# Optimization experiments

Hardware: AMD Instinct MI355X
Metric: run time of the kernel (lower is better)

## Reference

```python
import jax, jax.numpy as jnp
import numpy as np

H = 1024
E = 8
TOP_K = 2


def setup_inputs() -> dict:
    key = jax.random.key(0)
    ks = jax.random.split(key, 6)
    B, S = 4, 2048
    hidden_states = jax.random.normal(ks[0], (B, S, H), dtype=jnp.float32)
    # router weight, init N(0, 0.02)
    router_w = jax.random.normal(ks[1], (E, H), dtype=jnp.float32) * 0.02
    # stacked expert FFN params (nn.Linear: y = x @ W.T + b)
    lim = 1.0 / np.sqrt(H)
    W1 = jax.random.uniform(ks[2], (E, H, H), minval=-lim, maxval=lim, dtype=jnp.float32)
    b1 = jax.random.uniform(ks[3], (E, H), minval=-lim, maxval=lim, dtype=jnp.float32)
    W2 = jax.random.uniform(ks[4], (E, H, H), minval=-lim, maxval=lim, dtype=jnp.float32)
    b2 = jax.random.uniform(ks[5], (E, H), minval=-lim, maxval=lim, dtype=jnp.float32)
    return {"hidden_states": hidden_states, "router_w": router_w,
            "W1": W1, "b1": b1, "W2": W2, "b2": b2}


def reference(hidden_states, router_w, W1, b1, W2, b2):
    B, S, _ = hidden_states.shape
    # ---- router ----
    logits = jnp.einsum('bsh,eh->bse', hidden_states, router_w)  # [B,S,E]
    router_probs = jax.nn.softmax(logits.astype(jnp.float32), axis=-1)
    top_vals, top_idx = jax.lax.top_k(router_probs, TOP_K)        # [B,S,K]
    top_vals = top_vals / jnp.sum(top_vals, axis=-1, keepdims=True)  # norm_topk_prob
    # per-token per-expert combine weight (sum of top-k weights matching expert)
    w = jnp.sum(jax.nn.one_hot(top_idx, E, dtype=top_vals.dtype) * top_vals[..., None], axis=-2)  # [B,S,E]
    # ---- dense all-expert FFN (faithful to reference: every expert on every token) ----
    h1 = jax.nn.relu(jnp.einsum('bsh,efh->bsef', hidden_states, W1) + b1)   # [B,S,E,F]
    expert_out = jnp.einsum('bsef,egf->bseg', h1, W2) + b2                  # [B,S,E,H]
    moe_out = jnp.einsum('bseh,bse->bsh', expert_out, w)
    return hidden_states + moe_out, router_probs
```

## Files before the change

### kernel.cpp

```cpp
#include <hip/hip_runtime.h>
#include <hip/hip_bf16.h>


#define HD   1024
#define NTOK 8192
#define NEXP 8
#define BM   128
#define BN   256
#define BK   32
#define ZROW 8192
#define MAXP 17408
#define EP_LDSW 136

typedef __attribute__((ext_vector_type(8))) short  vshort8;
typedef __attribute__((ext_vector_type(4))) short  vshort4;
typedef __attribute__((ext_vector_type(4))) float  vfloat4;

typedef __attribute__((address_space(1))) const unsigned gas_uint;
typedef __attribute__((address_space(3))) unsigned       las_uint;

__device__ __forceinline__ void gld16(const void* g, void* l) {
    __builtin_amdgcn_global_load_lds((gas_uint*)g, (las_uint*)l, 16, 0, 0);
}

__device__ __forceinline__ short bf16r(float f) {
    union { float f; unsigned u; } a; a.f = f;
    unsigned r = a.u + 0x7FFFu + ((a.u >> 16) & 1u);
    return (short)(r >> 16);
}

__global__ void init_kernel(int* counts, int* fill, int* pair_token, short* xb) {
    int i = blockIdx.x * 256 + threadIdx.x;
    if (i < NEXP) { counts[i] = 0; fill[i] = 0; }
    if (i < MAXP) pair_token[i] = ZROW;
    if (i < HD / 8) {
        vshort8 z = {0, 0, 0, 0, 0, 0, 0, 0};
        *(vshort8*)(xb + (size_t)ZROW * HD + i * 8) = z;
    }
}

__global__ __launch_bounds__(256) void router_kernel(
    const float* __restrict__ x, const float* __restrict__ rw,
    float* __restrict__ out, short* __restrict__ xb,
    float* __restrict__ probs_out, int2* __restrict__ tok_top,
    float2* __restrict__ tok_w, int* __restrict__ counts) {
    __shared__ float rws[NEXP * HD];
    __shared__ int hist[NEXP];
    int t = threadIdx.x;
    if (t < NEXP) hist[t] = 0;
    for (int j = 0; j < 8; ++j) {
        int idx = j * 1024 + t * 4;
        *(vfloat4*)(rws + idx) = *(const vfloat4*)(rw + idx);
    }
    __syncthreads();
    int wave = t >> 6, lane = t & 63;
    for (int it = 0; it < 8; ++it) {
        int token = blockIdx.x * 32 + it * 4 + wave;
        const float* xr = x + (size_t)token * HD;
        float part[NEXP];
#pragma unroll
        for (int e = 0; e < NEXP; ++e) part[e] = 0.f;
        for (int j = 0; j < 4; ++j) {
            int off = j * 256 + lane * 4;
            vfloat4 xv = *(const vfloat4*)(xr + off);
            *(vfloat4*)(out + (size_t)token * HD + off) = xv;
            vshort4 bq;
            bq.x = bf16r(xv.x); bq.y = bf16r(xv.y); bq.z = bf16r(xv.z); bq.w = bf16r(xv.w);
            *(vshort4*)(xb + (size_t)token * HD + off) = bq;
#pragma unroll
            for (int e = 0; e < NEXP; ++e) {
                vfloat4 wv = *(const vfloat4*)(rws + e * HD + off);
                part[e] += xv.x * wv.x + xv.y * wv.y + xv.z * wv.z + xv.w * wv.w;
            }
        }
#pragma unroll
        for (int e = 0; e < NEXP; ++e)
            for (int off = 32; off; off >>= 1)
                part[e] += __shfl_xor(part[e], off, 64);
        if (lane == 0) {
            float m = part[0];
#pragma unroll
            for (int e = 1; e < NEXP; ++e) m = fmaxf(m, part[e]);
            float p[NEXP], s = 0.f;
#pragma unroll
            for (int e = 0; e < NEXP; ++e) { p[e] = expf(part[e] - m); s += p[e]; }
            float inv = 1.f / s;
#pragma unroll
            for (int e = 0; e < NEXP; ++e) {
                p[e] *= inv;
                probs_out[(size_t)token * NEXP + e] = p[e];
            }
            int i0 = 0;
#pragma unroll
            for (int e = 1; e < NEXP; ++e) if (p[e] > p[i0]) i0 = e;
            int i1 = (i0 == 0) ? 1 : 0;
#pragma unroll
            for (int e = 0; e < NEXP; ++e) if (e != i0 && p[e] > p[i1]) i1 = e;
            float s2 = 1.f / (p[i0] + p[i1]);
            tok_top[token] = make_int2(i0, i1);
            tok_w[token]   = make_float2(p[i0] * s2, p[i1] * s2);
            atomicAdd(&hist[i0], 1);
            atomicAdd(&hist[i1], 1);
        }
    }
    __syncthreads();
    if (t < NEXP) atomicAdd(&counts[t], hist[t]);
}

__global__ __launch_bounds__(256) void scatter_kernel(
    const int2* __restrict__ tok_top, const float2* __restrict__ tok_w,
    const int* __restrict__ counts, int* fill,
    int* __restrict__ pair_token, float* __restrict__ pair_w) {
    __shared__ int lhist[NEXP];
    __shared__ int lbase[NEXP];
    int t = threadIdx.x;
    if (t < NEXP) lhist[t] = 0;
    __syncthreads();
    int offs[NEXP];
    {
        int acc = 0;
#pragma unroll
        for (int f = 0; f < NEXP; ++f) {
            offs[f] = acc;
            acc += (counts[f] + 127) & ~127;
        }
    }
    int token = blockIdx.x * 256 + t;
    int2 ti = tok_top[token];
    float2 tw = tok_w[token];
    int r0 = atomicAdd(&lhist[ti.x], 1);
    int r1 = atomicAdd(&lhist[ti.y], 1);
    __syncthreads();
    if (t < NEXP) lbase[t] = atomicAdd(&fill[t], lhist[t]);
    __syncthreads();
    int s0 = offs[ti.x] + lbase[ti.x] + r0;
    pair_token[s0] = token; pair_w[s0] = tw.x;
    int s1 = offs[ti.y] + lbase[ti.y] + r1;
    pair_token[s1] = token; pair_w[s1] = tw.y;
}

__global__ void convw_kernel(const float* __restrict__ W1, const float* __restrict__ W2,
                             short* __restrict__ D1, short* __restrict__ D2) {
    size_t t = (size_t)blockIdx.x * 256 + threadIdx.x;
    const size_t PER = (size_t)NEXP * HD * HD / 8;
    const float* src = W1; short* dst = D1;
    if (t >= PER) { t -= PER; src = W2; dst = D2; }
    size_t C = t >> 6;
    int l  = (int)(t & 63);
    int kc = (int)(C & 31);
    int ng = (int)((C >> 5) & 63);
    int ei = (int)(C >> 11);
    int n = ng * 16 + (l & 15);
    int k = kc * 32 + (l >> 4) * 8;
    const float* s = src + ((size_t)ei * HD + n) * HD + k;
    vfloat4 a = *(const vfloat4*)s;
    vfloat4 b = *(const vfloat4*)(s + 4);
    vshort8 o;
    o[0] = bf16r(a.x); o[1] = bf16r(a.y); o[2] = bf16r(a.z); o[3] = bf16r(a.w);
    o[4] = bf16r(b.x); o[5] = bf16r(b.y); o[6] = bf16r(b.z); o[7] = bf16r(b.w);
    *(vshort8*)(dst + t * 8) = o;
}

template <int MODE>
__global__ __launch_bounds__(512, 4) void moe_gemm(
    const short* __restrict__ A, const short* __restrict__ Bw,
    const float* __restrict__ bias, const int* __restrict__ pair_token,
    const float* __restrict__ pair_w, const int* __restrict__ counts,
    short* __restrict__ h1sw_out, float* __restrict__ out) {
    __shared__ short smem[24576];

    const int row0 = blockIdx.x * BM;
    int e = 0;
    {
        int csum = 0;
#pragma unroll
        for (int f = 0; f < NEXP; ++f) {
            int p = (counts[f] + 127) & ~127;
            if (csum + p <= row0) e = f + 1;
            csum += p;
        }
        if (row0 >= csum) return;
    }

    const int t = threadIdx.x;
    const int wave = t >> 6, lane = t & 63;
    const int wm = wave >> 2, wn = wave & 3;
    const int quad = lane >> 4, l16 = lane & 15;
    const int colb = blockIdx.y * BN;

    const char* agp;
    if (MODE == 0) {
        int tok = pair_token[row0 + wave * 16 + l16];
        agp = (const char*)A + (size_t)tok * (HD * 2) + quad * 16;
    } else {
        agp = (const char*)A + ((size_t)(row0 >> 4) + wave) * 32768 + lane * 16;
    }
    const char* bgp = (const char*)Bw +
        ((size_t)e * 64 + (colb >> 4) + 2 * wave) * 32768 + lane * 16;

    vfloat4 acc[4][4];
#pragma unroll
    for (int i = 0; i < 4; ++i)
#pragma unroll
        for (int j = 0; j < 4; ++j)
            acc[i][j] = (vfloat4){0.f, 0.f, 0.f, 0.f};

#define STAGE(bsel, kt_)                                                      \
    {                                                                         \
        short* sa_ = smem + (bsel) * 4096;                                    \
        short* sb_ = smem + 8192 + (bsel) * 8192;                             \
        const char* ga_ = (MODE == 0)                                         \
            ? (agp + (size_t)(kt_) * 64)                                      \
            : (agp + (size_t)(kt_) * 1024);                                   \
        gld16(ga_, sa_ + wave * 512);                                         \
        gld16(bgp + (size_t)(kt_) * 1024,         sb_ + (2 * wave) * 512);    \
        gld16(bgp + 32768 + (size_t)(kt_) * 1024, sb_ + (2 * wave + 1) * 512);\
    }

    STAGE(0, 0)
    int cur = 0;
    for (int kt = 0; kt < HD / BK; ++kt) {
        if (kt < HD / BK - 1) {
            STAGE(cur ^ 1, kt + 1)
            asm volatile("s_waitcnt vmcnt(3)" ::: "memory");
        } else {
            asm volatile("s_waitcnt vmcnt(0)" ::: "memory");
        }
        __builtin_amdgcn_s_barrier();
        asm volatile("" ::: "memory");
        const short* sa = smem + cur * 4096;
        const short* sb = smem + 8192 + cur * 8192;
        vshort8 af[4], bfr[4];
#pragma unroll
        for (int i = 0; i < 4; ++i)
            af[i] = *(const vshort8*)(sa + (wm * 4 + i) * 512 + lane * 8);
#pragma unroll
        for (int j = 0; j < 4; ++j)
            bfr[j] = *(const vshort8*)(sb + (wn * 4 + j) * 512 + lane * 8);
#pragma unroll
        for (int i = 0; i < 4; ++i)
#pragma unroll
            for (int j = 0; j < 4; ++j)
                acc[i][j] = __builtin_amdgcn_mfma_f32_16x16x32_bf16(af[i], bfr[j], acc[i][j], 0, 0, 0);
        asm volatile("" ::: "memory");
        __builtin_amdgcn_s_barrier();
        cur ^= 1;
    }
#undef STAGE

    if (MODE == 0) {
        __syncthreads();
#pragma unroll
        for (int h = 0; h < 2; ++h) {
            if ((wn >> 1) == h) {
#pragma unroll
                for (int j = 0; j < 4; ++j) {
                    int col = (wn & 1) * 64 + j * 16 + l16;
                    float bv = bias[e * HD + colb + h * 128 + col];
#pragma unroll
                    for (int i = 0; i < 4; ++i) {
                        int rl = wm * 64 + i * 16 + quad * 4;
#pragma unroll
                        for (int reg = 0; reg < 4; ++reg) {
                            float v = acc[i][j][reg] + bv;
                            v = v > 0.f ? v : 0.f;
                            smem[(rl + reg) * EP_LDSW + col] = bf16r(v);
                        }
                    }
                }
            }
            __syncthreads();
            int lrow = wave * 16 + l16;
#pragma unroll
            for (int kk = 0; kk < 4; ++kk) {
                vshort8 v = *(const vshort8*)(smem + lrow * EP_LDSW + kk * 32 + quad * 8);
                size_t chunk = ((size_t)((row0 >> 4) + wave) * 32) + (colb >> 5) + h * 4 + kk;
                *(vshort8*)(h1sw_out + chunk * 512 + lane * 8) = v;
            }
            if (h == 0) __syncthreads();
        }
    } else {
        int tok[4][4]; float wv[4][4];
#pragma unroll
        for (int i = 0; i < 4; ++i)
#pragma unroll
            for (int reg = 0; reg < 4; ++reg) {
                int r = row0 + wm * 64 + i * 16 + quad * 4 + reg;
                tok[i][reg] = pair_token[r];
                wv[i][reg] = pair_w[r];
            }
#pragma unroll
        for (int j = 0; j < 4; ++j) {
            int col = colb + wn * 64 + j * 16 + l16;
            float bv = bias[e * HD + col];
#pragma unroll
            for (int i = 0; i < 4; ++i)
#pragma unroll
                for (int reg = 0; reg < 4; ++reg)
                    if (tok[i][reg] < ZROW)
                        atomicAdd(out + (size_t)tok[i][reg] * HD + col,
                                  wv[i][reg] * (acc[i][j][reg] + bv));
        }
    }
}

extern "C" void kernel_launch(void* const* d_in, const int* in_sizes, int n_in,
                              void* d_out, int out_size, void* d_ws, size_t ws_size,
                              hipStream_t stream) {
    const float* x  = (const float*)d_in[0];
    const float* rw = (const float*)d_in[1];
    const float* W1 = (const float*)d_in[2];
    const float* b1 = (const float*)d_in[3];
    const float* W2 = (const float*)d_in[4];
    const float* b2 = (const float*)d_in[5];
    float* out   = (float*)d_out;
    float* probs = out + (size_t)NTOK * HD;

    char* ws = (char*)d_ws;
    short* xb = (short*)ws;            ws += (size_t)(NTOK + 1) * HD * 2;
    short* h1 = (short*)ws;            ws += (size_t)MAXP * HD * 2;
    int*   pair_token = (int*)ws;      ws += MAXP * 4;
    float* pair_w     = (float*)ws;    ws += MAXP * 4;
    int*   counts = (int*)ws;          ws += 256;
    int*   fill   = (int*)ws;          ws += 256;
    int2*   tok_top = (int2*)ws;       ws += NTOK * 8;
    float2* tok_w   = (float2*)ws;     ws += NTOK * 8;
    short* w1sw = (short*)ws;          ws += (size_t)NEXP * HD * HD * 2;
    short* w2sw = (short*)ws;          ws += (size_t)NEXP * HD * HD * 2;
    (void)ws_size;

    init_kernel<<<MAXP / 256, 256, 0, stream>>>(counts, fill, pair_token, xb);
    router_kernel<<<NTOK / 32, 256, 0, stream>>>(x, rw, out, xb, probs,
                                                 tok_top, tok_w, counts);
    scatter_kernel<<<NTOK / 256, 256, 0, stream>>>(tok_top, tok_w, counts, fill,
                                                   pair_token, pair_w);
    int cg = (int)(2 * ((size_t)NEXP * HD * HD / 8) / 256);
    convw_kernel<<<cg, 256, 0, stream>>>(W1, W2, w1sw, w2sw);
    dim3 gg(MAXP / BM, HD / BN);
    moe_gemm<0><<<gg, 512, 0, stream>>>(xb, w1sw, b1, pair_token, pair_w, counts, h1, nullptr);
    moe_gemm<1><<<gg, 512, 0, stream>>>(h1, w2sw, b2, pair_token, pair_w, counts, nullptr, out);
}
```

Baseline: 313.0 us.

## Shrink GEMM tile to 128x128 with 4 waves and triple-buffered LDS register prefetch

Changes the MoE GEMM tile from 128x256 with 8 waves to 128x128 with 4 waves, so each wave now stages two A and two B chunks per k-step. The main loop becomes a three-buffer LDS pipeline unrolled by six, with register double-buffered fragments: fragments for the next k-step are read from LDS while the MFMAs for the current step run, and there is one barrier per step instead of two. The aim is to hide LDS and global latency and to double the number of column blocks for better occupancy. The trade-off is lower B reuse per block, more A traffic, and manual pipeline bookkeeping that depends on the fixed 32 k-steps.

```diff
diff --git a/kernel.cpp b/kernel.cpp
--- a/kernel.cpp
+++ b/kernel.cpp
@@ -6,7 +6,7 @@
 #define NTOK 8192
 #define NEXP 8
 #define BM   128
-#define BN   256
+#define BN   128
 #define BK   32
 #define ZROW 8192
 #define MAXP 17408
@@ -162,7 +162,7 @@
 }
 
 template <int MODE>
-__global__ __launch_bounds__(512, 4) void moe_gemm(
+__global__ __launch_bounds__(256, 3) void moe_gemm(
     const short* __restrict__ A, const short* __restrict__ Bw,
     const float* __restrict__ bias, const int* __restrict__ pair_token,
     const float* __restrict__ pair_w, const int* __restrict__ counts,
@@ -184,19 +184,23 @@
 
     const int t = threadIdx.x;
     const int wave = t >> 6, lane = t & 63;
-    const int wm = wave >> 2, wn = wave & 3;
+    const int wm = wave >> 1, wn = wave & 1;
     const int quad = lane >> 4, l16 = lane & 15;
     const int colb = blockIdx.y * BN;
 
-    const char* agp;
+    const char *agp0, *agp1;
     if (MODE == 0) {
-        int tok = pair_token[row0 + wave * 16 + l16];
-        agp = (const char*)A + (size_t)tok * (HD * 2) + quad * 16;
+        int tok0 = pair_token[row0 + (2 * wave) * 16 + l16];
+        int tok1 = pair_token[row0 + (2 * wave + 1) * 16 + l16];
+        agp0 = (const char*)A + (size_t)tok0 * (HD * 2) + quad * 16;
+        agp1 = (const char*)A + (size_t)tok1 * (HD * 2) + quad * 16;
     } else {
-        agp = (const char*)A + ((size_t)(row0 >> 4) + wave) * 32768 + lane * 16;
-    }
-    const char* bgp = (const char*)Bw +
+        agp0 = (const char*)A + ((size_t)(row0 >> 4) + 2 * wave) * 32768 + lane * 16;
+        agp1 = (const char*)A + ((size_t)(row0 >> 4) + 2 * wave + 1) * 32768 + lane * 16;
+    }
+    const char* bgp0 = (const char*)Bw +
         ((size_t)e * 64 + (colb >> 4) + 2 * wave) * 32768 + lane * 16;
+    const char* bgp1 = bgp0 + 32768;
 
     vfloat4 acc[4][4];
 #pragma unroll
@@ -205,79 +209,103 @@
         for (int j = 0; j < 4; ++j)
             acc[i][j] = (vfloat4){0.f, 0.f, 0.f, 0.f};
 
+    vshort8 afA[4], bfA[4], afB[4], bfB[4];
+
 #define STAGE(bsel, kt_)                                                      \
     {                                                                         \
-        short* sa_ = smem + (bsel) * 4096;                                    \
-        short* sb_ = smem + 8192 + (bsel) * 8192;                             \
-        const char* ga_ = (MODE == 0)                                         \
-            ? (agp + (size_t)(kt_) * 64)                                      \
-            : (agp + (size_t)(kt_) * 1024);                                   \
-        gld16(ga_, sa_ + wave * 512);                                         \
-        gld16(bgp + (size_t)(kt_) * 1024,         sb_ + (2 * wave) * 512);    \
-        gld16(bgp + 32768 + (size_t)(kt_) * 1024, sb_ + (2 * wave + 1) * 512);\
+        short* s_ = smem + (bsel) * 8192;                                     \
+        const char* a0_ = (MODE == 0) ? (agp0 + (size_t)(kt_) * 64)           \
+                                      : (agp0 + (size_t)(kt_) * 1024);        \
+        const char* a1_ = (MODE == 0) ? (agp1 + (size_t)(kt_) * 64)           \
+                                      : (agp1 + (size_t)(kt_) * 1024);        \
+        gld16(a0_, s_ + (2 * wave) * 512);                                    \
+        gld16(a1_, s_ + (2 * wave + 1) * 512);                                \
+        gld16(bgp0 + (size_t)(kt_) * 1024, s_ + 4096 + (2 * wave) * 512);     \
+        gld16(bgp1 + (size_t)(kt_) * 1024, s_ + 4096 + (2 * wave + 1) * 512); \
+    }
+
+#define LOADFRAGS(af_, bf_, bsel)                                             \
+    {                                                                         \
+        const short* sa_ = smem + (bsel) * 8192;                              \
+        _Pragma("unroll")                                                     \
+        for (int i = 0; i < 4; ++i)                                           \
+            af_[i] = *(const vshort8*)(sa_ + (wm * 4 + i) * 512 + lane * 8);  \
+        _Pragma("unroll")                                                     \
+        for (int j = 0; j < 4; ++j)                                           \
+            bf_[j] = *(const vshort8*)(sa_ + 4096 + (wn * 4 + j) * 512 + lane * 8); \
+    }
+
+#define DOMFMA(af_, bf_)                                                      \
+    {                                                                         \
+        _Pragma("unroll")                                                     \
+        for (int i = 0; i < 4; ++i)                                           \
+            _Pragma("unroll")                                                 \
+            for (int j = 0; j < 4; ++j)                                       \
+                acc[i][j] = __builtin_amdgcn_mfma_f32_16x16x32_bf16(          \
+                    af_[i], bf_[j], acc[i][j], 0, 0, 0);                      \
+    }
+
+#define BODY(sbuf, rbuf, ktp2, AFc, BFc, AFr, BFr)                            \
+    {                                                                         \
+        STAGE(sbuf, ktp2)                                                     \
+        asm volatile("s_waitcnt vmcnt(4) lgkmcnt(0)" ::: "memory");           \
+        __builtin_amdgcn_s_barrier();                                         \
+        LOADFRAGS(AFr, BFr, rbuf)                                             \
+        DOMFMA(AFc, BFc)                                                      \
     }
 
     STAGE(0, 0)
-    int cur = 0;
-    for (int kt = 0; kt < HD / BK; ++kt) {
-        if (kt < HD / BK - 1) {
-            STAGE(cur ^ 1, kt + 1)
-            asm volatile("s_waitcnt vmcnt(3)" ::: "memory");
-        } else {
-            asm volatile("s_waitcnt vmcnt(0)" ::: "memory");
-        }
-        __builtin_amdgcn_s_barrier();
-        asm volatile("" ::: "memory");
-        const short* sa = smem + cur * 4096;
-        const short* sb = smem + 8192 + cur * 8192;
-        vshort8 af[4], bfr[4];
-#pragma unroll
-        for (int i = 0; i < 4; ++i)
-            af[i] = *(const vshort8*)(sa + (wm * 4 + i) * 512 + lane * 8);
-#pragma unroll
-        for (int j = 0; j < 4; ++j)
-            bfr[j] = *(const vshort8*)(sb + (wn * 4 + j) * 512 + lane * 8);
-#pragma unroll
-        for (int i = 0; i < 4; ++i)
-#pragma unroll
-            for (int j = 0; j < 4; ++j)
-                acc[i][j] = __builtin_amdgcn_mfma_f32_16x16x32_bf16(af[i], bfr[j], acc[i][j], 0, 0, 0);
-        asm volatile("" ::: "memory");
-        __builtin_amdgcn_s_barrier();
-        cur ^= 1;
-    }
+    STAGE(1, 1)
+    asm volatile("s_waitcnt vmcnt(4)" ::: "memory");
+    __builtin_amdgcn_s_barrier();
+    LOADFRAGS(afA, bfA, 0)
+
+    for (int kt = 0; kt < 30; kt += 6) {
+        BODY(2, 1, kt + 2, afA, bfA, afB, bfB)
+        BODY(0, 2, kt + 3, afB, bfB, afA, bfA)
+        BODY(1, 0, kt + 4, afA, bfA, afB, bfB)
+        BODY(2, 1, kt + 5, afB, bfB, afA, bfA)
+        BODY(0, 2, kt + 6, afA, bfA, afB, bfB)
+        BODY(1, 0, kt + 7, afB, bfB, afA, bfA)
+    }
+    asm volatile("s_waitcnt vmcnt(0) lgkmcnt(0)" ::: "memory");
+    __builtin_amdgcn_s_barrier();
+    LOADFRAGS(afB, bfB, 1)
+    DOMFMA(afA, bfA)
+    DOMFMA(afB, bfB)
+
+#undef BODY
+#undef DOMFMA
+#undef LOADFRAGS
 #undef STAGE
 
     if (MODE == 0) {
         __syncthreads();
 #pragma unroll
-        for (int h = 0; h < 2; ++h) {
-            if ((wn >> 1) == h) {
-#pragma unroll
-                for (int j = 0; j < 4; ++j) {
-                    int col = (wn & 1) * 64 + j * 16 + l16;
-                    float bv = bias[e * HD + colb + h * 128 + col];
-#pragma unroll
-                    for (int i = 0; i < 4; ++i) {
-                        int rl = wm * 64 + i * 16 + quad * 4;
-#pragma unroll
-                        for (int reg = 0; reg < 4; ++reg) {
-                            float v = acc[i][j][reg] + bv;
-                            v = v > 0.f ? v : 0.f;
-                            smem[(rl + reg) * EP_LDSW + col] = bf16r(v);
-                        }
-                    }
+        for (int j = 0; j < 4; ++j) {
+            int col = wn * 64 + j * 16 + l16;
+            float bv = bias[e * HD + colb + col];
+#pragma unroll
+            for (int i = 0; i < 4; ++i) {
+                int rl = wm * 64 + i * 16 + quad * 4;
+#pragma unroll
+                for (int reg = 0; reg < 4; ++reg) {
+                    float v = acc[i][j][reg] + bv;
+                    v = v > 0.f ? v : 0.f;
+                    smem[(rl + reg) * EP_LDSW + col] = bf16r(v);
                 }
             }
-            __syncthreads();
-            int lrow = wave * 16 + l16;
+        }
+        __syncthreads();
+#pragma unroll
+        for (int p = 0; p < 2; ++p) {
+            int lrow = p * 64 + wave * 16 + l16;
 #pragma unroll
             for (int kk = 0; kk < 4; ++kk) {
                 vshort8 v = *(const vshort8*)(smem + lrow * EP_LDSW + kk * 32 + quad * 8);
-                size_t chunk = ((size_t)((row0 >> 4) + wave) * 32) + (colb >> 5) + h * 4 + kk;
+                size_t chunk = ((size_t)(row0 >> 4) + p * 4 + wave) * 32 + (colb >> 5) + kk;
                 *(vshort8*)(h1sw_out + chunk * 512 + lane * 8) = v;
             }
-            if (h == 0) __syncthreads();
         }
     } else {
         int tok[4][4]; float wv[4][4];
@@ -337,6 +365,6 @@
     int cg = (int)(2 * ((size_t)NEXP * HD * HD / 8) / 256);
     convw_kernel<<<cg, 256, 0, stream>>>(W1, W2, w1sw, w2sw);
     dim3 gg(MAXP / BM, HD / BN);
-    moe_gemm<0><<<gg, 512, 0, stream>>>(xb, w1sw, b1, pair_token, pair_w, counts, h1, nullptr);
-    moe_gemm<1><<<gg, 512, 0, stream>>>(h1, w2sw, b2, pair_token, pair_w, counts, nullptr, out);
-}
+    moe_gemm<0><<<gg, 256, 0, stream>>>(xb, w1sw, b1, pair_token, pair_w, counts, h1, nullptr);
+    moe_gemm<1><<<gg, 256, 0, stream>>>(h1, w2sw, b2, pair_token, pair_w, counts, nullptr, out);
+}
```

Result: no change. 312.6 us (-0.2%).
